# Optimization experiments

Measured on AMD Instinct MI355X. Metric: run time of the kernel, lower is better.

## Reference

```python
import jax, jax.numpy as jnp
import numpy as np

N, E = 3200, 50000
RBF, HID = 16, 128
CUT = 5.0
NS, NV = 32, 16            # multiplicities of 0e and 1o blocks
D = NS + 3 * NV            # 80 = node/message irrep dim
WNUM = NS*NS + NV*NS + NS*NV + NV*NV  # 2304 tensor-product weights per edge
EPS = 1e-8
# path normalization (fully-connected TP, 2 paths per output irrep)
A1 = 1.0 / np.sqrt(2.0 * NS)
A2 = 1.0 / np.sqrt(2.0 * NV)
A3 = 1.0 / np.sqrt(2.0 * NS)
A4 = 1.0 / np.sqrt(2.0 * NV)
ISQ3 = 1.0 / np.sqrt(3.0)


def setup_inputs() -> dict:
    key = jax.random.key(0)
    ks = jax.random.split(key, 24)
    nrm = lambda k, s, sc=1.0: jax.random.normal(k, s, jnp.float32) * sc
    x = nrm(ks[0], (N, D))
    edge_src = jax.random.randint(ks[1], (E,), 0, N)
    edge_dst = jax.random.randint(ks[2], (E,), 0, N)
    dirs = nrm(ks[3], (E, 3))
    unit = dirs / jnp.linalg.norm(dirs, axis=1, keepdims=True)
    # component-normalized SH for l=0,1: [1, sqrt(3)*r_hat]
    edge_sh = jnp.concatenate([jnp.ones((E, 1), jnp.float32), np.sqrt(3.0) * unit], axis=1)
    edge_rbf = nrm(ks[4], (E, RBF))
    edge_len = jax.random.uniform(ks[5], (E,), jnp.float32, 0.1, 6.0)  # some beyond cutoff
    inp = dict(x=x, edge_src=edge_src, edge_dst=edge_dst, edge_sh=edge_sh,
               edge_rbf=edge_rbf, edge_len=edge_len)
    # IrrepNorm affine params
    inp['norm_w'] = jnp.ones((D,), jnp.float32)
    inp['norm_b'] = jnp.zeros((D,), jnp.float32)
    # radial weight MLP (RBF -> HID -> HID -> WNUM)
    inp['mw1'] = nrm(ks[6], (RBF, HID), 1.0/np.sqrt(RBF)); inp['mb1'] = jnp.zeros((HID,), jnp.float32)
    inp['mw2'] = nrm(ks[7], (HID, HID), 1.0/np.sqrt(HID)); inp['mb2'] = jnp.zeros((HID,), jnp.float32)
    inp['mw3'] = nrm(ks[8], (HID, WNUM), 1.0/np.sqrt(HID)); inp['mb3'] = jnp.zeros((WNUM,), jnp.float32)
    # edge gate MLP (RBF -> HID -> 1)
    inp['gw1'] = nrm(ks[9], (RBF, HID), 1.0/np.sqrt(RBF)); inp['gb1'] = jnp.zeros((HID,), jnp.float32)
    inp['gw2'] = nrm(ks[10], (HID, 1), 1.0/np.sqrt(HID)); inp['gb2'] = jnp.zeros((1,), jnp.float32)
    # equivariant linears (e3nn stores N(0,1) weights, normalizes by 1/sqrt(fan_in))
    inp['Ws'] = nrm(ks[11], (NS, NS + NV))   # msg_linear scalar part: 32 -> 32 scalars + 16 gates
    inp['Wv'] = nrm(ks[12], (NV, NV))        # msg_linear vector part
    inp['Us'] = nrm(ks[13], (NS, NS))        # update_linear
    inp['Uv'] = nrm(ks[14], (NV, NV))
    inp['Ss'] = nrm(ks[15], (NS, NS))        # self_linear
    inp['Sv'] = nrm(ks[16], (NV, NV))
    inp['res_scale'] = jnp.float32(0.1)
    return inp


def _irrep_norm(x, w, b):
    s = x[:, :NS]
    v = x[:, NS:].reshape(-1, NV, 3)
    mean = s.mean(axis=1, keepdims=True)
    var = ((s - mean) ** 2).mean(axis=1, keepdims=True)
    s = (s - mean) / jnp.sqrt(var + EPS)
    rms = jnp.sqrt((v ** 2).mean(axis=2, keepdims=True) + EPS)
    v = v / rms
    out = jnp.concatenate([s, v.reshape(-1, 3 * NV)], axis=-1)
    return out * w + b


def reference(x, edge_src, edge_dst, edge_sh, edge_rbf, edge_len,
              norm_w, norm_b, mw1, mb1, mw2, mb2, mw3, mb3,
              gw1, gb1, gw2, gb2, Ws, Wv, Us, Uv, Ss, Sv, res_scale):
    silu = jax.nn.silu
    x_norm = _irrep_norm(x, norm_w, norm_b)                  # [N, 80]
    # radial tensor-product weights per edge
    h = silu(edge_rbf @ mw1 + mb1)
    h = silu(h @ mw2 + mb2)
    tpw = h @ mw3 + mb3                                      # [E, 2304]
    o1 = NS*NS; o2 = o1 + NV*NS; o3 = o2 + NS*NV
    w1 = tpw[:, :o1].reshape(-1, NS, NS)
    w2 = tpw[:, o1:o2].reshape(-1, NV, NS)
    w3 = tpw[:, o2:o3].reshape(-1, NS, NV)
    w4 = tpw[:, o3:].reshape(-1, NV, NV)
    # gather source node features
    xs = x_norm[edge_src, :NS]                               # [E, 32]
    xv = x_norm[edge_src, NS:].reshape(-1, NV, 3)            # [E, 16, 3]
    sh0 = edge_sh[:, 0]                                      # [E]
    sh1 = edge_sh[:, 1:4]                                    # [E, 3]
    # fully-connected TP paths
    msg_s = A1 * jnp.einsum('ei,eio->eo', xs * sh0[:, None], w1)
    inner = jnp.einsum('eim,em->ei', xv, sh1) * ISQ3         # 1o x 1o -> 0e
    msg_s = msg_s + A2 * jnp.einsum('ei,eio->eo', inner, w2)
    msg_v = A3 * jnp.einsum('ei,eio->eo', xs, w3)[:, :, None] * sh1[:, None, :]
    msg_v = msg_v + A4 * jnp.einsum('eim,eio->eom', xv, w4) * sh0[:, None, None]
    m = jnp.concatenate([msg_s, msg_v.reshape(-1, 3 * NV)], axis=-1)  # [E, 80]
    # cutoff envelope and learned edge gate
    cutoff_w = 0.5 * (jnp.cos(jnp.pi * edge_len / CUT) + 1.0) * (edge_len <= CUT).astype(x.dtype)
    gate_w = jax.nn.sigmoid(silu(edge_rbf @ gw1 + gb1) @ gw2 + gb2)   # [E, 1]
    edge_w = cutoff_w[:, None] * gate_w                               # [E, 1]
    m = m * edge_w
    # scatter-add aggregate + normalization
    agg = jax.ops.segment_sum(m, edge_dst, num_segments=N)            # [N, 80]
    den = jax.ops.segment_sum(edge_w, edge_dst, num_segments=N)       # [N, 1]
    agg = agg / jnp.maximum(den, 1e-8)
    # msg_linear -> scalars + gates + gated vectors
    ag_s = agg[:, :NS]
    ag_v = agg[:, NS:].reshape(-1, NV, 3)
    sc = (ag_s @ Ws) / np.sqrt(NS)                                    # [N, 48]
    vc = jnp.einsum('nim,io->nom', ag_v, Wv) / np.sqrt(NV)            # [N, 16, 3]
    s_g = silu(sc[:, :NS])
    gates = jax.nn.sigmoid(sc[:, NS:])
    v_g = vc * gates[:, :, None]
    # update + self interaction
    upd_s = (s_g @ Us) / np.sqrt(NS)
    upd_v = jnp.einsum('nim,io->nom', v_g, Uv) / np.sqrt(NV)
    self_s = (x_norm[:, :NS] @ Ss) / np.sqrt(NS)
    self_v = jnp.einsum('nim,io->nom', x_norm[:, NS:].reshape(-1, NV, 3), Sv) / np.sqrt(NV)
    out = jnp.concatenate([self_s + upd_s, (self_v + upd_v).reshape(-1, 3 * NV)], axis=-1)
    return x + res_scale * out
```

## Files before the change

kernel.cpp:

```cpp
#include <hip/hip_runtime.h>
#include <hip/hip_bf16.h>
#include <math.h>

#define N_NODES 3200
#define E_EDGES 50000
#define RBFN 16
#define HID 128
#define NS 32
#define NV 16
#define DD 80
#define WNUM 2304
#define CUTF 5.0f
#define EPSF 1e-8f

#define A1C 0.125f
#define A2C 0.17677669529663687f
#define A3C 0.125f
#define A4C 0.17677669529663687f
#define A2ISQ 0.10206207261596575f

typedef __attribute__((ext_vector_type(4))) float f32x4;
typedef __attribute__((ext_vector_type(8))) short bf16x8;

__device__ __forceinline__ float sigm(float x) { return 1.0f / (1.0f + __expf(-x)); }
__device__ __forceinline__ float silu_f(float x) { return x * sigm(x); }

__device__ __forceinline__ short bf16r(float x) {
    union { float f; unsigned u; } v; v.f = x;
    unsigned r = (v.u + 0x7fffu + ((v.u >> 16) & 1u)) >> 16;
    return (short)r;
}
__device__ __forceinline__ float b2f(unsigned short s) {
    union { float f; unsigned u; } v; v.u = ((unsigned)s) << 16; return v.f;
}

__global__ void k_scan(const int* __restrict__ hist, int* __restrict__ start) {
    __shared__ int part[256];
    int t = threadIdx.x;
    int loc[13];
    int s = 0;
#pragma unroll
    for (int j = 0; j < 13; j++) {
        int idx = t * 13 + j;
        int v = (idx < N_NODES) ? hist[idx] : 0;
        loc[j] = s; s += v;
    }
    part[t] = s;
    __syncthreads();
    for (int off = 1; off < 256; off <<= 1) {
        int v = part[t];
        int add = (t >= off) ? part[t - off] : 0;
        __syncthreads();
        part[t] = v + add;
        __syncthreads();
    }
    int pre = (t == 0) ? 0 : part[t - 1];
#pragma unroll
    for (int j = 0; j < 13; j++) {
        int idx = t * 13 + j;
        if (idx < N_NODES) start[idx] = pre + loc[j];
    }
    if (t == 255) start[N_NODES] = part[255];
}

__global__ void k_scatter(const int* __restrict__ edst, const int* __restrict__ start,
                          int* __restrict__ cur, int* __restrict__ perm) {
    int e = blockIdx.x * 256 + threadIdx.x;
    if (e < E_EDGES) {
        int d = edst[e];
        int pos = start[d] + atomicAdd(&cur[d], 1);
        perm[pos] = e;
    }
}

__global__ void k_prep0(const float* __restrict__ mw2, __hip_bfloat16* __restrict__ mw2f) {
    __shared__ __hip_bfloat16 st[2048];
    int t = blockIdx.x, tid = threadIdx.x;
    for (int idx = tid; idx < 2048; idx += 256) {
        int k = idx >> 4, c = idx & 15;
        float v = mw2[k * HID + t * 16 + c];
        int kk = k >> 5, q4 = (k >> 3) & 3, j = k & 7;
        st[kk * 512 + (q4 * 16 + c) * 8 + j] = __float2bfloat16(v);
    }
    __syncthreads();
    ((bf16x8*)(mw2f + t * 2048))[tid] = ((const bf16x8*)st)[tid];
}

__global__ __launch_bounds__(256) void k_front(
    const float* __restrict__ rbf, const float* __restrict__ elen,
    const int* __restrict__ edst,
    const float* __restrict__ mw1, const float* __restrict__ mb1,
    const float* __restrict__ gw1, const float* __restrict__ gb1,
    const float* __restrict__ gw2, const float* __restrict__ gb2,
    const float* __restrict__ mb2, const __hip_bfloat16* __restrict__ mw2f,
    const float* __restrict__ mw3, const float* __restrict__ mb3,
    const float* __restrict__ x, const float* __restrict__ nw, const float* __restrict__ nb,
    float* __restrict__ ewg, __hip_bfloat16* __restrict__ h2b,
    __hip_bfloat16* __restrict__ mw3f, __hip_bfloat16* __restrict__ biasf,
    float* __restrict__ xn, int* __restrict__ hist) {
    __shared__ __align__(16) char smem[16640];
    int b = blockIdx.x, tid = threadIdx.x;
    if (b < 782) {
        __hip_bfloat16* h1l = (__hip_bfloat16*)smem;
        int wid = __builtin_amdgcn_readfirstlane(tid >> 6);
        int lane = tid & 63;
        int base = b * 64;
        int eb = base + wid * 16;
        {
            int c0 = lane, c1 = 64 + lane;
            float t0[16], t1[16], g0[16], g1[16];
            float b0 = mb1[c0], b1 = mb1[c1], gb0v = gb1[c0], gb1v = gb1[c1];
#pragma unroll
            for (int e = 0; e < 16; e++) { t0[e] = b0; t1[e] = b1; g0[e] = gb0v; g1[e] = gb1v; }
#pragma unroll
            for (int r = 0; r < RBFN; r++) {
                float w0 = mw1[r * HID + c0], w1 = mw1[r * HID + c1];
                float v0 = gw1[r * HID + c0], v1 = gw1[r * HID + c1];
#pragma unroll
                for (int e = 0; e < 16; e++) {
                    int ee = eb + e; if (ee >= E_EDGES) ee = E_EDGES - 1;
                    float rv = rbf[ee * RBFN + r];
                    t0[e] += rv * w0; t1[e] += rv * w1;
                    g0[e] += rv * v0; g1[e] += rv * v1;
                }
            }
            float q0 = gw2[c0], q1 = gw2[c1];
            float gb2v = gb2[0];
#pragma unroll
            for (int e = 0; e < 16; e++) {
                int le = wid * 16 + e;
                h1l[le * 128 + c0] = __float2bfloat16(silu_f(t0[e]));
                h1l[le * 128 + c1] = __float2bfloat16(silu_f(t1[e]));
                float p = silu_f(g0[e]) * q0 + silu_f(g1[e]) * q1;
                p += __shfl_xor(p, 1);  p += __shfl_xor(p, 2);  p += __shfl_xor(p, 4);
                p += __shfl_xor(p, 8);  p += __shfl_xor(p, 16); p += __shfl_xor(p, 32);
                if (lane == 0 && eb + e < E_EDGES) {
                    float len = elen[eb + e];
                    float cut = (len <= CUTF) ? 0.5f * (cosf(3.14159265358979f * len / CUTF) + 1.0f) : 0.f;
                    ewg[eb + e] = cut * sigm(p + gb2v);
                }
            }
        }
        __syncthreads();
        {
            int q4 = lane >> 4, l15 = lane & 15;
            int le = wid * 16 + l15;
            bf16x8 af[4];
#pragma unroll
            for (int kk = 0; kk < 4; kk++)
                af[kk] = *(const bf16x8*)(h1l + le * 128 + kk * 32 + q4 * 8);
            const f32x4 zf = {0.f, 0.f, 0.f, 0.f};
#pragma unroll
            for (int ct = 0; ct < 8; ct++) {
                f32x4 acc = zf;
#pragma unroll
                for (int kk = 0; kk < 4; kk++) {
                    bf16x8 bw = *(const bf16x8*)(mw2f + (ct * 4 + kk) * 512 + lane * 8);
                    acc = __builtin_amdgcn_mfma_f32_16x16x32_bf16(af[kk], bw, acc, 0, 0, 0);
                }
                float bias = mb2[ct * 16 + l15];
#pragma unroll
                for (int r = 0; r < 4; r++) {
                    int ge = base + wid * 16 + q4 * 4 + r;
                    if (ge < E_EDGES)
                        h2b[ge * HID + ct * 16 + l15] = __float2bfloat16(silu_f(acc[r] + bias));
                }
            }
        }
    } else if (b < 927) {
        int b2 = b - 782;
        __hip_bfloat16* st = (__hip_bfloat16*)smem;
        if (b2 < 144) {
            for (int idx = tid; idx < 2048; idx += 256) {
                int k = idx >> 4, c = idx & 15;
                float v = mw3[k * WNUM + b2 * 16 + c];
                int kk = k >> 5, q4 = (k >> 3) & 3, j = k & 7;
                st[kk * 512 + (q4 * 16 + c) * 8 + j] = __float2bfloat16(v);
            }
            __syncthreads();
            ((bf16x8*)(mw3f + b2 * 2048))[tid] = ((const bf16x8*)st)[tid];
        } else {
            for (int idx = tid; idx < 3072; idx += 256) {
                float val;
                if (idx < 1024) {
                    int oh = idx >> 9, l = (idx >> 3) & 63, j = idx & 7;
                    int o = oh * 16 + (l & 15), i = (l >> 4) * 8 + j;
                    val = mb3[i * 32 + o];
                } else if (idx < 2048) {
                    int t = idx - 1024;
                    int oh = t >> 9, l = (t >> 3) & 63, j = t & 7;
                    int o = oh * 16 + (l & 15), i = (l >> 4) * 8 + j;
                    val = (i < 16) ? mb3[1024 + i * 32 + o] : 0.f;
                } else if (idx < 2560) {
                    int t = idx - 2048;
                    int l = t >> 3, j = t & 7;
                    int o = l & 15, i = (l >> 4) * 8 + j;
                    val = mb3[1536 + i * 16 + o];
                } else {
                    int t = idx - 2560;
                    int l = t >> 3, j = t & 7;
                    int o = l & 15, i = (l >> 4) * 8 + j;
                    val = (i < 16) ? mb3[2048 + i * 16 + o] : 0.f;
                }
                biasf[idx] = __float2bfloat16(val);
            }
        }
    } else if (b < 1727) {
        float* row = (float*)smem;
        int sub = tid >> 6, t = tid & 63;
        int n = (b - 927) * 4 + sub;
        float* rw = row + sub * 80;
        const float* xr = x + n * DD;
        rw[t] = xr[t];
        if (t < 16) rw[64 + t] = xr[64 + t];
        __syncthreads();
        float mean = 0.f;
#pragma unroll
        for (int i = 0; i < NS; i++) mean += rw[i];
        mean *= (1.0f / NS);
        float var = 0.f;
#pragma unroll
        for (int i = 0; i < NS; i++) { float d = rw[i] - mean; var += d * d; }
        var *= (1.0f / NS);
        float inv = rsqrtf(var + EPSF);
        if (t < NS) xn[n * DD + t] = (rw[t] - mean) * inv * nw[t] + nb[t];
        if (t < 48) {
            int j = t / 3;
            float v0 = rw[NS + 3 * j], v1 = rw[NS + 3 * j + 1], v2 = rw[NS + 3 * j + 2];
            float rms = sqrtf((v0 * v0 + v1 * v1 + v2 * v2) * (1.0f / 3.0f) + EPSF);
            xn[n * DD + NS + t] = rw[NS + t] / rms * nw[NS + t] + nb[NS + t];
        }
    } else {
        int e = (b - 1727) * 256 + tid;
        if (e < E_EDGES) atomicAdd(&hist[edst[e]], 1);
    }
}

__global__ __launch_bounds__(128) void k_msg(
    const float* __restrict__ xn, const __hip_bfloat16* __restrict__ h2b,
    const float* __restrict__ ewg, const int* __restrict__ esrc,
    const int* __restrict__ edst, const int* __restrict__ perm,
    const float* __restrict__ esh,
    const __hip_bfloat16* __restrict__ mw3f, const __hip_bfloat16* __restrict__ biasf,
    const int* __restrict__ startp, float* __restrict__ agg, float* __restrict__ den) {
    __shared__ __align__(16) char pool[29696];
    unsigned short (*xng)[82]  = (unsigned short(*)[82])(pool);
    unsigned short (*innr)[16] = (unsigned short(*)[16])(pool + 20992);
    float (*sh1l)[4] = (float(*)[4])(pool + 25088);
    float* sh0l = (float*)(pool + 27136);
    float* ewl  = (float*)(pool + 27648);
    int* dstl   = (int*)(pool + 28160);
    int* srcl   = (int*)(pool + 28672);
    int* gel    = (int*)(pool + 29184);
    float* msgl = (float*)pool;

    const int tid = threadIdx.x;
    const int wid = __builtin_amdgcn_readfirstlane(tid >> 6);
    const int lane = tid & 63;
    const int q4 = lane >> 4;
    const int l15 = lane & 15;
    const int ib = q4 * 8;
    const int role = blockIdx.x & 1;
    const int e0 = (blockIdx.x >> 1) * 128;

    if (tid < 128) {
        int slot = e0 + tid;
        bool v = slot < E_EDGES;
        int ge = v ? perm[slot] : 0;
        gel[tid] = ge;
        srcl[tid] = esrc[ge];
        dstl[tid] = v ? edst[ge] : -1;
        ewl[tid] = v ? ewg[ge] : 0.f;
        sh0l[tid] = esh[ge * 4];
        sh1l[tid][0] = esh[ge * 4 + 1];
        sh1l[tid][1] = esh[ge * 4 + 2];
        sh1l[tid][2] = esh[ge * 4 + 3];
    }
    __syncthreads();
    for (int idx = tid; idx < 128 * 80; idx += 128) {
        int e = idx / 80, q = idx - e * 80;
        xng[e][q] = (unsigned short)bf16r(xn[srcl[e] * 80 + q]);
    }
    __syncthreads();
    for (int idx = tid; idx < 128 * 16; idx += 128) {
        int e = idx >> 4, i = idx & 15;
        float d = b2f(xng[e][32 + 3 * i]) * sh1l[e][0]
                + b2f(xng[e][32 + 3 * i + 1]) * sh1l[e][1]
                + b2f(xng[e][32 + 3 * i + 2]) * sh1l[e][2];
        innr[e][i] = (unsigned short)bf16r(A2ISQ * d);
    }
    __syncthreads();

    int el[4];
#pragma unroll
    for (int et = 0; et < 4; et++) el[et] = wid * 64 + et * 16 + l15;
    bf16x8 hfr[4][4];
#pragma unroll
    for (int et = 0; et < 4; et++) {
        int ge = gel[el[et]];
        const __hip_bfloat16* hr = h2b + ge * HID;
#pragma unroll
        for (int kk = 0; kk < 4; kk++)
            hfr[et][kk] = *(const bf16x8*)(hr + kk * 32 + ib);
    }
    const f32x4 zf = {0.f, 0.f, 0.f, 0.f};
    const bf16x8* gp = (const bf16x8*)mw3f;
    int cnt = E_EDGES - e0; if (cnt > 128) cnt = 128;

    if (role == 0) {
        float f1[4];
        f32x4 msgS[2][4];
#pragma unroll
        for (int et = 0; et < 4; et++) {
            f1[et] = A1C * sh0l[el[et]];
            bf16x8 p18, p28;
#pragma unroll
            for (int j = 0; j < 8; j++) {
                p18[j] = bf16r(b2f(xng[el[et]][ib + j]) * f1[et]);
                p28[j] = (ib + j < 16) ? (short)innr[el[et]][ib + j] : (short)0;
            }
            bf16x8 ba1a = *(const bf16x8*)(biasf + lane * 8);
            bf16x8 ba1b = *(const bf16x8*)(biasf + 512 + lane * 8);
            bf16x8 ba2a = *(const bf16x8*)(biasf + 1024 + lane * 8);
            bf16x8 ba2b = *(const bf16x8*)(biasf + 1536 + lane * 8);
            f32x4 a0 = __builtin_amdgcn_mfma_f32_16x16x32_bf16(ba1a, p18, zf, 0, 0, 0);
            msgS[0][et] = __builtin_amdgcn_mfma_f32_16x16x32_bf16(ba2a, p28, a0, 0, 0, 0);
            f32x4 a1 = __builtin_amdgcn_mfma_f32_16x16x32_bf16(ba1b, p18, zf, 0, 0, 0);
            msgS[1][et] = __builtin_amdgcn_mfma_f32_16x16x32_bf16(ba2b, p28, a1, 0, 0, 0);
        }
        auto computeA = [&](int n, bf16x8 (&A)[8]) {
            f32x4 acc[2][4];
#pragma unroll
            for (int half = 0; half < 2; half++)
#pragma unroll
                for (int et = 0; et < 4; et++) acc[half][et] = zf;
#pragma unroll
            for (int half = 0; half < 2; half++)
#pragma unroll
                for (int kk = 0; kk < 4; kk++)
#pragma unroll
                    for (int et = 0; et < 4; et++)
                        acc[half][et] = __builtin_amdgcn_mfma_f32_16x16x32_bf16(
                            A[half * 4 + kk], hfr[et][kk], acc[half][et], 0, 0, 0);
            float p[4];
            if (n < 32) {
#pragma unroll
                for (int et = 0; et < 4; et++) p[et] = f1[et] * b2f(xng[el[et]][n]);
            } else {
#pragma unroll
                for (int et = 0; et < 4; et++) p[et] = b2f(innr[el[et]][n - 32]);
            }
#pragma unroll
            for (int half = 0; half < 2; half++)
#pragma unroll
                for (int et = 0; et < 4; et++)
#pragma unroll
                    for (int r = 0; r < 4; r++)
                        msgS[half][et][r] += p[et] * acc[half][et][r];
        };
        bf16x8 A0[8], A1[8];
#pragma unroll
        for (int f = 0; f < 8; f++) A0[f] = gp[f * 64 + lane];
        for (int n = 0; n < 48; n += 2) {
            const bf16x8* g1 = gp + (n + 1) * 512;
#pragma unroll
            for (int f = 0; f < 8; f++) A1[f] = g1[f * 64 + lane];
            computeA(n, A0);
            if (n + 2 < 48) {
                const bf16x8* g2 = gp + (n + 2) * 512;
#pragma unroll
                for (int f = 0; f < 8; f++) A0[f] = g2[f * 64 + lane];
            }
            computeA(n + 1, A1);
        }
        __syncthreads();
#pragma unroll
        for (int et = 0; et < 4; et++) {
            int le = el[et];
            float ew = ewl[le];
#pragma unroll
            for (int oh = 0; oh < 2; oh++)
#pragma unroll
                for (int r = 0; r < 4; r++)
                    msgl[le * 48 + oh * 16 + q4 * 4 + r] = msgS[oh][et][r] * ew;
        }
        __syncthreads();
        if (tid < 33) {
            int c = tid;
            int cur = dstl[0];
            float acc = 0.f;
            for (int r = 0; r < cnt; r++) {
                int nd = dstl[r];
                if (nd != cur) {
                    if (cur >= 0) {
                        bool interior = (startp[cur] >= e0) && (startp[cur + 1] <= e0 + 128);
                        float* p = (c == 32) ? (den + cur) : (agg + cur * 80 + c);
                        if (interior) *p = acc; else atomicAdd(p, acc);
                    }
                    acc = 0.f; cur = nd;
                }
                acc += (c == 32) ? ewl[r] : msgl[r * 48 + c];
            }
            if (cur >= 0) {
                bool interior = (startp[cur] >= e0) && (startp[cur + 1] <= e0 + 128);
                float* p = (c == 32) ? (den + cur) : (agg + cur * 80 + c);
                if (interior) *p = acc; else atomicAdd(p, acc);
            }
        }
    } else {
        float f4e[4];
        f32x4 q3[4], qv[3][4];
#pragma unroll
        for (int et = 0; et < 4; et++) {
            f4e[et] = A4C * sh0l[el[et]];
            bf16x8 xs8;
#pragma unroll
            for (int j = 0; j < 8; j++) xs8[j] = (short)xng[el[et]][ib + j];
            bf16x8 ba3 = *(const bf16x8*)(biasf + 2048 + lane * 8);
            bf16x8 ba4 = *(const bf16x8*)(biasf + 2560 + lane * 8);
            q3[et] = __builtin_amdgcn_mfma_f32_16x16x32_bf16(ba3, xs8, zf, 0, 0, 0);
#pragma unroll
            for (int m = 0; m < 3; m++) {
                bf16x8 t8;
#pragma unroll
                for (int j = 0; j < 8; j++) {
                    int i = ib + j;
                    t8[j] = (i < 16) ? (short)xng[el[et]][32 + 3 * i + m] : (short)0;
                }
                qv[m][et] = __builtin_amdgcn_mfma_f32_16x16x32_bf16(ba4, t8, zf, 0, 0, 0);
            }
        }
        auto computeB = [&](int n, bf16x8 (&A)[8]) {
            f32x4 acc[2][4];
#pragma unroll
            for (int half = 0; half < 2; half++)
#pragma unroll
                for (int et = 0; et < 4; et++) acc[half][et] = zf;
#pragma unroll
            for (int half = 0; half < 2; half++)
#pragma unroll
                for (int kk = 0; kk < 4; kk++)
#pragma unroll
                    for (int et = 0; et < 4; et++)
                        acc[half][et] = __builtin_amdgcn_mfma_f32_16x16x32_bf16(
                            A[half * 4 + kk], hfr[et][kk], acc[half][et], 0, 0, 0);
            if (n < 64) {
#pragma unroll
                for (int half = 0; half < 2; half++) {
                    int i = 2 * (n - 48) + half;
                    float p[4];
#pragma unroll
                    for (int et = 0; et < 4; et++) p[et] = b2f(xng[el[et]][i]);
#pragma unroll
                    for (int et = 0; et < 4; et++)
#pragma unroll
                        for (int r = 0; r < 4; r++)
                            q3[et][r] += p[et] * acc[half][et][r];
                }
            } else {
#pragma unroll
                for (int half = 0; half < 2; half++) {
                    int i = 2 * (n - 64) + half;
#pragma unroll
                    for (int m = 0; m < 3; m++) {
                        float p[4];
#pragma unroll
                        for (int et = 0; et < 4; et++) p[et] = b2f(xng[el[et]][32 + 3 * i + m]);
#pragma unroll
                        for (int et = 0; et < 4; et++)
#pragma unroll
                            for (int r = 0; r < 4; r++)
                                qv[m][et][r] += p[et] * acc[half][et][r];
                    }
                }
            }
        };
        bf16x8 A0[8], A1[8];
#pragma unroll
        for (int f = 0; f < 8; f++) A0[f] = gp[48 * 512 + f * 64 + lane];
        for (int n = 48; n < 72; n += 2) {
            const bf16x8* g1 = gp + (n + 1) * 512;
#pragma unroll
            for (int f = 0; f < 8; f++) A1[f] = g1[f * 64 + lane];
            computeB(n, A0);
            if (n + 2 < 72) {
                const bf16x8* g2 = gp + (n + 2) * 512;
#pragma unroll
                for (int f = 0; f < 8; f++) A0[f] = g2[f * 64 + lane];
            }
            computeB(n + 1, A1);
        }
        __syncthreads();
#pragma unroll
        for (int et = 0; et < 4; et++) {
            int le = el[et];
            float ew = ewl[le];
            float s0 = sh1l[le][0], s1 = sh1l[le][1], s2 = sh1l[le][2];
            float b4 = f4e[et];
#pragma unroll
            for (int r = 0; r < 4; r++) {
                int o = q4 * 4 + r;
                float qq = A3C * q3[et][r];
                msgl[le * 48 + o * 3 + 0] = (qq * s0 + b4 * qv[0][et][r]) * ew;
                msgl[le * 48 + o * 3 + 1] = (qq * s1 + b4 * qv[1][et][r]) * ew;
                msgl[le * 48 + o * 3 + 2] = (qq * s2 + b4 * qv[2][et][r]) * ew;
            }
        }
        __syncthreads();
        if (tid < 48) {
            int c = tid;
            int cur = dstl[0];
            float acc = 0.f;
            for (int r = 0; r < cnt; r++) {
                int nd = dstl[r];
                if (nd != cur) {
                    if (cur >= 0) {
                        bool interior = (startp[cur] >= e0) && (startp[cur + 1] <= e0 + 128);
                        float* p = agg + cur * 80 + 32 + c;
                        if (interior) *p = acc; else atomicAdd(p, acc);
                    }
                    acc = 0.f; cur = nd;
                }
                acc += msgl[r * 48 + c];
            }
            if (cur >= 0) {
                bool interior = (startp[cur] >= e0) && (startp[cur + 1] <= e0 + 128);
                float* p = agg + cur * 80 + 32 + c;
                if (interior) *p = acc; else atomicAdd(p, acc);
            }
        }
    }
}

__global__ void k_update(
    const float* __restrict__ x, const float* __restrict__ xn,
    const float* __restrict__ agg, const float* __restrict__ den,
    const float* __restrict__ Ws, const float* __restrict__ Wv,
    const float* __restrict__ Us, const float* __restrict__ Uv,
    const float* __restrict__ Ss, const float* __restrict__ Sv,
    const float* __restrict__ rsp, float* __restrict__ out) {
    int n = blockIdx.x, t = threadIdx.x;
    __shared__ float ag[DD];
    __shared__ float xnl[DD];
    __shared__ float sg[NS];
    __shared__ float gt[NV];
    __shared__ float vg[48];
    float idv = 1.0f / fmaxf(den[n], 1e-8f);
    ag[t] = agg[n * DD + t] * idv;
    if (t < 16) ag[64 + t] = agg[n * DD + 64 + t] * idv;
    xnl[t] = xn[n * DD + t];
    if (t < 16) xnl[64 + t] = xn[n * DD + 64 + t];
    __syncthreads();
    const float iqs = 0.17677669529663687f;
    const float iqv = 0.25f;
    if (t < 48) {
        float acc = 0.f;
#pragma unroll
        for (int i = 0; i < NS; i++) acc += ag[i] * Ws[i * 48 + t];
        acc *= iqs;
        if (t < NS) sg[t] = silu_f(acc);
        else gt[t - NS] = sigm(acc);
    }
    __syncthreads();
    if (t < 48) {
        int o = t / 3, m = t - 3 * o;
        float acc = 0.f;
#pragma unroll
        for (int i = 0; i < NV; i++) acc += ag[NS + 3 * i + m] * Wv[i * NV + o];
        vg[t] = acc * iqv * gt[o];
    }
    __syncthreads();
    float rs = rsp[0];
    if (t < NS) {
        float us = 0.f, ss = 0.f;
#pragma unroll
        for (int i = 0; i < NS; i++) { us += sg[i] * Us[i * NS + t]; ss += xnl[i] * Ss[i * NS + t]; }
        out[n * DD + t] = x[n * DD + t] + rs * ((ss + us) * iqs);
    }
    if (t < 48) {
        int o = t / 3, m = t - 3 * o;
        float uv = 0.f, sv = 0.f;
#pragma unroll
        for (int i = 0; i < NV; i++) { uv += vg[3 * i + m] * Uv[i * NV + o]; sv += xnl[NS + 3 * i + m] * Sv[i * NV + o]; }
        out[n * DD + NS + t] = x[n * DD + NS + t] + rs * ((sv + uv) * iqv);
    }
}

extern "C" void kernel_launch(void* const* d_in, const int* in_sizes, int n_in,
                              void* d_out, int out_size, void* d_ws, size_t ws_size,
                              hipStream_t stream) {
    (void)in_sizes; (void)n_in; (void)out_size; (void)ws_size;
    const float* x    = (const float*)d_in[0];
    const int*   esrc = (const int*)d_in[1];
    const int*   edst = (const int*)d_in[2];
    const float* esh  = (const float*)d_in[3];
    const float* erbf = (const float*)d_in[4];
    const float* elen = (const float*)d_in[5];
    const float* nw   = (const float*)d_in[6];
    const float* nb   = (const float*)d_in[7];
    const float* mw1  = (const float*)d_in[8];
    const float* mb1  = (const float*)d_in[9];
    const float* mw2  = (const float*)d_in[10];
    const float* mb2  = (const float*)d_in[11];
    const float* mw3  = (const float*)d_in[12];
    const float* mb3  = (const float*)d_in[13];
    const float* gw1  = (const float*)d_in[14];
    const float* gb1  = (const float*)d_in[15];
    const float* gw2  = (const float*)d_in[16];
    const float* gb2  = (const float*)d_in[17];
    const float* Ws   = (const float*)d_in[18];
    const float* Wv   = (const float*)d_in[19];
    const float* Us   = (const float*)d_in[20];
    const float* Uv   = (const float*)d_in[21];
    const float* Ss   = (const float*)d_in[22];
    const float* Sv   = (const float*)d_in[23];
    const float* rsp  = (const float*)d_in[24];
    float* out = (float*)d_out;
    float* ws  = (float*)d_ws;

    float* agg    = ws;
    float* den    = ws + 256000;
    int*   hist   = (int*)(ws + 259200);
    int*   cur    = (int*)(ws + 262400);
    int*   startp = (int*)(ws + 265600);
    int*   perm   = (int*)(ws + 268801);
    float* xn     = ws + 318804;
    float* ewg    = ws + 574804;
    __hip_bfloat16* h2b   = (__hip_bfloat16*)(ws + 624804);
    __hip_bfloat16* mw3f  = (__hip_bfloat16*)(ws + 3824804);
    __hip_bfloat16* biasf = (__hip_bfloat16*)(ws + 3972260);
    __hip_bfloat16* mw2f  = (__hip_bfloat16*)(ws + 3973796);

    hipMemsetAsync(ws, 0, 265600 * sizeof(float), stream);
    k_prep0<<<8, 256, 0, stream>>>(mw2, mw2f);
    k_front<<<1923, 256, 0, stream>>>(erbf, elen, edst, mw1, mb1, gw1, gb1, gw2, gb2,
                                      mb2, mw2f, mw3, mb3, x, nw, nb,
                                      ewg, h2b, mw3f, biasf, xn, hist);
    k_scan<<<1, 256, 0, stream>>>(hist, startp);
    k_scatter<<<196, 256, 0, stream>>>(edst, startp, cur, perm);
    k_msg<<<782, 128, 0, stream>>>(xn, h2b, ewg, esrc, edst, perm, esh,
                                   mw3f, biasf, startp, agg, den);
    k_update<<<N_NODES, 64, 0, stream>>>(x, xn, agg, den, Ws, Wv, Us, Uv, Ss, Sv, rsp, out);
}
```

Baseline: 269.3 us.

## Split scalar-output message work across two blocks per edge tile

```diff
diff --git a/kernel.cpp b/kernel.cpp
--- a/kernel.cpp
+++ b/kernel.cpp
@@ -260,8 +260,9 @@
     const int q4 = lane >> 4;
     const int l15 = lane & 15;
     const int ib = q4 * 8;
-    const int role = blockIdx.x & 1;
-    const int e0 = (blockIdx.x >> 1) * 128;
+    const int grp = blockIdx.x / 3;
+    const int role = blockIdx.x - grp * 3;
+    const int e0 = grp * 128;
 
     if (tid < 128) {
         int slot = e0 + tid;
@@ -282,12 +283,14 @@
         xng[e][q] = (unsigned short)bf16r(xn[srcl[e] * 80 + q]);
     }
     __syncthreads();
-    for (int idx = tid; idx < 128 * 16; idx += 128) {
-        int e = idx >> 4, i = idx & 15;
-        float d = b2f(xng[e][32 + 3 * i]) * sh1l[e][0]
-                + b2f(xng[e][32 + 3 * i + 1]) * sh1l[e][1]
-                + b2f(xng[e][32 + 3 * i + 2]) * sh1l[e][2];
-        innr[e][i] = (unsigned short)bf16r(A2ISQ * d);
+    if (role == 1) {
+        for (int idx = tid; idx < 128 * 16; idx += 128) {
+            int e = idx >> 4, i = idx & 15;
+            float d = b2f(xng[e][32 + 3 * i]) * sh1l[e][0]
+                    + b2f(xng[e][32 + 3 * i + 1]) * sh1l[e][1]
+                    + b2f(xng[e][32 + 3 * i + 2]) * sh1l[e][2];
+            innr[e][i] = (unsigned short)bf16r(A2ISQ * d);
+        }
     }
     __syncthreads();
 
@@ -307,28 +310,45 @@
     const bf16x8* gp = (const bf16x8*)mw3f;
     int cnt = E_EDGES - e0; if (cnt > 128) cnt = 128;
 
-    if (role == 0) {
+    if (role <= 1) {
         float f1[4];
         f32x4 msgS[2][4];
 #pragma unroll
         for (int et = 0; et < 4; et++) {
             f1[et] = A1C * sh0l[el[et]];
-            bf16x8 p18, p28;
-#pragma unroll
-            for (int j = 0; j < 8; j++) {
-                p18[j] = bf16r(b2f(xng[el[et]][ib + j]) * f1[et]);
-                p28[j] = (ib + j < 16) ? (short)innr[el[et]][ib + j] : (short)0;
-            }
-            bf16x8 ba1a = *(const bf16x8*)(biasf + lane * 8);
-            bf16x8 ba1b = *(const bf16x8*)(biasf + 512 + lane * 8);
-            bf16x8 ba2a = *(const bf16x8*)(biasf + 1024 + lane * 8);
-            bf16x8 ba2b = *(const bf16x8*)(biasf + 1536 + lane * 8);
-            f32x4 a0 = __builtin_amdgcn_mfma_f32_16x16x32_bf16(ba1a, p18, zf, 0, 0, 0);
-            msgS[0][et] = __builtin_amdgcn_mfma_f32_16x16x32_bf16(ba2a, p28, a0, 0, 0, 0);
-            f32x4 a1 = __builtin_amdgcn_mfma_f32_16x16x32_bf16(ba1b, p18, zf, 0, 0, 0);
-            msgS[1][et] = __builtin_amdgcn_mfma_f32_16x16x32_bf16(ba2b, p28, a1, 0, 0, 0);
-        }
-        auto computeA = [&](int n, bf16x8 (&A)[8]) {
+            msgS[0][et] = zf; msgS[1][et] = zf;
+        }
+        if (role == 0) {
+#pragma unroll
+            for (int et = 0; et < 4; et++) {
+                bf16x8 p18, p28;
+#pragma unroll
+                for (int j = 0; j < 8; j++) {
+                    p18[j] = bf16r(b2f(xng[el[et]][ib + j]) * f1[et]);
+                    p28[j] = 0;
+                }
+#pragma unroll
+                for (int j = 0; j < 8; j++) {
+                    int i = ib + j;
+                    if (i < 16) {
+                        int le = el[et];
+                        float d = b2f(xng[le][32 + 3 * i]) * sh1l[le][0]
+                                + b2f(xng[le][32 + 3 * i + 1]) * sh1l[le][1]
+                                + b2f(xng[le][32 + 3 * i + 2]) * sh1l[le][2];
+                        p28[j] = bf16r(A2ISQ * d);
+                    }
+                }
+                bf16x8 ba1a = *(const bf16x8*)(biasf + lane * 8);
+                bf16x8 ba1b = *(const bf16x8*)(biasf + 512 + lane * 8);
+                bf16x8 ba2a = *(const bf16x8*)(biasf + 1024 + lane * 8);
+                bf16x8 ba2b = *(const bf16x8*)(biasf + 1536 + lane * 8);
+                f32x4 a0 = __builtin_amdgcn_mfma_f32_16x16x32_bf16(ba1a, p18, zf, 0, 0, 0);
+                msgS[0][et] = __builtin_amdgcn_mfma_f32_16x16x32_bf16(ba2a, p28, a0, 0, 0, 0);
+                f32x4 a1 = __builtin_amdgcn_mfma_f32_16x16x32_bf16(ba1b, p18, zf, 0, 0, 0);
+                msgS[1][et] = __builtin_amdgcn_mfma_f32_16x16x32_bf16(ba2b, p28, a1, 0, 0, 0);
+            }
+        }
+        auto computeS = [&](int n, bf16x8 (&A)[8]) {
             f32x4 acc[2][4];
 #pragma unroll
             for (int half = 0; half < 2; half++)
@@ -358,20 +378,22 @@
                     for (int r = 0; r < 4; r++)
                         msgS[half][et][r] += p[et] * acc[half][et][r];
         };
+        const int n0 = role * 24;
+        const int n1 = n0 + 24;
         bf16x8 A0[8], A1[8];
 #pragma unroll
-        for (int f = 0; f < 8; f++) A0[f] = gp[f * 64 + lane];
-        for (int n = 0; n < 48; n += 2) {
+        for (int f = 0; f < 8; f++) A0[f] = gp[n0 * 512 + f * 64 + lane];
+        for (int n = n0; n < n1; n += 2) {
             const bf16x8* g1 = gp + (n + 1) * 512;
 #pragma unroll
             for (int f = 0; f < 8; f++) A1[f] = g1[f * 64 + lane];
-            computeA(n, A0);
-            if (n + 2 < 48) {
+            computeS(n, A0);
+            if (n + 2 < n1) {
                 const bf16x8* g2 = gp + (n + 2) * 512;
 #pragma unroll
                 for (int f = 0; f < 8; f++) A0[f] = g2[f * 64 + lane];
             }
-            computeA(n + 1, A1);
+            computeS(n + 1, A1);
         }
         __syncthreads();
 #pragma unroll
@@ -385,7 +407,8 @@
                     msgl[le * 48 + oh * 16 + q4 * 4 + r] = msgS[oh][et][r] * ew;
         }
         __syncthreads();
-        if (tid < 33) {
+        int nch = (role == 0) ? 33 : 32;
+        if (tid < nch) {
             int c = tid;
             int cur = dstl[0];
             float acc = 0.f;
@@ -393,18 +416,24 @@
                 int nd = dstl[r];
                 if (nd != cur) {
                     if (cur >= 0) {
-                        bool interior = (startp[cur] >= e0) && (startp[cur + 1] <= e0 + 128);
-                        float* p = (c == 32) ? (den + cur) : (agg + cur * 80 + c);
-                        if (interior) *p = acc; else atomicAdd(p, acc);
+                        if (c == 32) {
+                            bool interior = (startp[cur] >= e0) && (startp[cur + 1] <= e0 + 128);
+                            if (interior) den[cur] = acc; else atomicAdd(den + cur, acc);
+                        } else {
+                            atomicAdd(agg + cur * 80 + c, acc);
+                        }
                     }
                     acc = 0.f; cur = nd;
                 }
                 acc += (c == 32) ? ewl[r] : msgl[r * 48 + c];
             }
             if (cur >= 0) {
-                bool interior = (startp[cur] >= e0) && (startp[cur + 1] <= e0 + 128);
-                float* p = (c == 32) ? (den + cur) : (agg + cur * 80 + c);
-                if (interior) *p = acc; else atomicAdd(p, acc);
+                if (c == 32) {
+                    bool interior = (startp[cur] >= e0) && (startp[cur + 1] <= e0 + 128);
+                    if (interior) den[cur] = acc; else atomicAdd(den + cur, acc);
+                } else {
+                    atomicAdd(agg + cur * 80 + c, acc);
+                }
             }
         }
     } else {
@@ -430,7 +459,7 @@
                 qv[m][et] = __builtin_amdgcn_mfma_f32_16x16x32_bf16(ba4, t8, zf, 0, 0, 0);
             }
         }
-        auto computeB = [&](int n, bf16x8 (&A)[8]) {
+        auto computeV = [&](int n, bf16x8 (&A)[8]) {
             f32x4 acc[2][4];
 #pragma unroll
             for (int half = 0; half < 2; half++)
@@ -482,13 +511,13 @@
             const bf16x8* g1 = gp + (n + 1) * 512;
 #pragma unroll
             for (int f = 0; f < 8; f++) A1[f] = g1[f * 64 + lane];
-            computeB(n, A0);
+            computeV(n, A0);
             if (n + 2 < 72) {
                 const bf16x8* g2 = gp + (n + 2) * 512;
 #pragma unroll
                 for (int f = 0; f < 8; f++) A0[f] = g2[f * 64 + lane];
             }
-            computeB(n + 1, A1);
+            computeV(n + 1, A1);
         }
         __syncthreads();
 #pragma unroll
@@ -638,7 +667,7 @@
                                       ewg, h2b, mw3f, biasf, xn, hist);
     k_scan<<<1, 256, 0, stream>>>(hist, startp);
     k_scatter<<<196, 256, 0, stream>>>(edst, startp, cur, perm);
-    k_msg<<<782, 128, 0, stream>>>(xn, h2b, ewg, esrc, edst, perm, esh,
-                                   mw3f, biasf, startp, agg, den);
+    k_msg<<<1173, 128, 0, stream>>>(xn, h2b, ewg, esrc, edst, perm, esh,
+                                    mw3f, biasf, startp, agg, den);
     k_update<<<N_NODES, 64, 0, stream>>>(x, xn, agg, den, Ws, Wv, Us, Uv, Ss, Sv, rsp, out);
 }
```

New measurement: 270.5 us. No clear change (+0.5%).
